# Performance work log

Measured on AMD Instinct MI355X. Metric: run time of the kernel, lower is better.

Reference implementation:

```python
import jax, jax.numpy as jnp
import numpy as np

B, L, D = 8192, 200, 64
NUM_ITEMS = 100000
HID = 64  # attention hidden_dim


def setup_inputs() -> dict:
    key = jax.random.key(0)
    ks = jax.random.split(key, 16)
    inp = {
        "item_sequence": jax.random.randint(ks[0], (B, L), 0, NUM_ITEMS),
        "click_sequence": jax.random.randint(ks[1], (B, L), 0, 2),
        "seq_length": jax.random.randint(ks[2], (B, 1), 1, L + 1),
        "target_item": jax.random.randint(ks[3], (B, 1), 0, NUM_ITEMS),
        "context_features": jax.random.normal(ks[4], (B, 9), dtype=jnp.float32),
        # embedding table (num_items+1, D)
        "emb_table": jax.random.normal(ks[5], (NUM_ITEMS + 1, D), dtype=jnp.float32) * 0.05,
        # attention MLP: Linear(2D->64), Linear(64->32), Linear(32->1)
        "aw1": jax.random.normal(ks[6], (2 * D, HID), dtype=jnp.float32) * 0.05,
        "ab1": jnp.zeros((HID,), jnp.float32),
        "aw2": jax.random.normal(ks[7], (HID, HID // 2), dtype=jnp.float32) * 0.05,
        "ab2": jnp.zeros((HID // 2,), jnp.float32),
        "aw3": jax.random.normal(ks[8], (HID // 2, 1), dtype=jnp.float32) * 0.05,
        "ab3": jnp.zeros((1,), jnp.float32),
        # context MLP: Linear(9->32)
        "cw": jax.random.normal(ks[9], (9, 32), dtype=jnp.float32) * 0.05,
        "cb": jnp.zeros((32,), jnp.float32),
        # head MLP: Linear(160->128), Linear(128->64), Linear(64->1)
        "mw1": jax.random.normal(ks[10], (2 * D + 32, 128), dtype=jnp.float32) * 0.05,
        "mb1": jnp.zeros((128,), jnp.float32),
        "mw2": jax.random.normal(ks[11], (128, 64), dtype=jnp.float32) * 0.05,
        "mb2": jnp.zeros((64,), jnp.float32),
        "mw3": jax.random.normal(ks[12], (64, 1), dtype=jnp.float32) * 0.05,
        "mb3": jnp.zeros((1,), jnp.float32),
    }
    return inp


def reference(item_sequence, click_sequence, seq_length, target_item, context_features,
              emb_table, aw1, ab1, aw2, ab2, aw3, ab3, cw, cb,
              mw1, mb1, mw2, mb2, mw3, mb3):
    seq_emb = emb_table[item_sequence]                 # [B, L, D]
    tgt_emb = emb_table[target_item[:, 0]]             # [B, D]
    seq_len = item_sequence.shape[1]
    mask = (jnp.arange(seq_len)[None, :] < seq_length).astype(seq_emb.dtype)  # [B, L]

    # DIN attention: concat(query, keys) -> 3-layer MLP -> masked softmax -> weighted sum
    q = jnp.broadcast_to(tgt_emb[:, None, :], seq_emb.shape)          # [B, L, D]
    att_in = jnp.concatenate([q, seq_emb], axis=-1)                   # [B, L, 2D]
    h = jax.nn.relu(att_in @ aw1 + ab1)
    h = jax.nn.relu(h @ aw2 + ab2)
    scores = (h @ aw3 + ab3)[..., 0]                                  # [B, L]
    scores = jnp.where(mask == 0, jnp.asarray(-1e9, scores.dtype), scores)
    w = jax.nn.softmax(scores, axis=1)                                # [B, L]
    attended = jnp.einsum('bl,bld->bd', w, seq_emb)                   # [B, D]

    ctx = jax.nn.relu(context_features @ cw + cb)                     # [B, 32]
    comb = jnp.concatenate([attended, tgt_emb, ctx], axis=1)          # [B, 2D+32]
    h = jax.nn.relu(comb @ mw1 + mb1)
    h = jax.nn.relu(h @ mw2 + mb2)
    out = jax.nn.sigmoid(h @ mw3 + mb3)[:, 0]                         # [B]
    return out
```

## Files before the change

kernel.cpp:

```cpp
#include <hip/hip_runtime.h>
#include <cmath>

typedef __attribute__((ext_vector_type(8))) short s16x8;
typedef __attribute__((ext_vector_type(4))) short s16x4;
typedef __attribute__((ext_vector_type(4))) float f32x4;

__device__ __forceinline__ short f2bf(float f) {
    union { float f; unsigned u; } v; v.f = f;
    unsigned r = v.u + 0x7FFFu + ((v.u >> 16) & 1u);
    return (short)(r >> 16);
}
__device__ __forceinline__ float bf2f(short s) {
    union { unsigned u; float f; } v; v.u = ((unsigned)(unsigned short)s) << 16;
    return v.f;
}
__device__ __forceinline__ s16x8 cvt8(float4 a, float4 b) {
    s16x8 r = { f2bf(a.x), f2bf(a.y), f2bf(a.z), f2bf(a.w),
                f2bf(b.x), f2bf(b.y), f2bf(b.z), f2bf(b.w) };
    return r;
}

#define W1SEQ_SH  0
#define W1TOP_SH  4096
#define W2_SH     8192
#define MW1T_SH   10240
#define MW2T_SH   30720
#define QC_F      19456
#define CB_SH     1087488

__global__ __launch_bounds__(256)
void din_wprep_kernel(const float* __restrict__ aw1,
                      const float* __restrict__ aw2,
                      const float* __restrict__ mw1,
                      const float* __restrict__ mw2,
                      short* __restrict__ ws)
{
    const int wb = blockIdx.x;
    const int t = threadIdx.x;
    if (wb == 0) {
        for (int idx = t; idx < 4096; idx += 256) {
            int j = idx & 7, lane = (idx >> 3) & 63, fr = idx >> 9;
            int n = (fr >> 1) * 16 + (lane & 15);
            int k = (fr & 1) * 32 + (lane >> 4) * 8 + j;
            ws[W1SEQ_SH + idx] = f2bf(aw1[(64 + k) * 64 + n]);
        }
    } else if (wb == 1) {
        for (int idx = t; idx < 4096; idx += 256) {
            int j = idx & 7, lane = (idx >> 3) & 63, fr = idx >> 9;
            int n = (fr >> 1) * 16 + (lane & 15);
            int k = (fr & 1) * 32 + (lane >> 4) * 8 + j;
            ws[W1TOP_SH + idx] = f2bf(aw1[k * 64 + n]);
        }
    } else if (wb == 2) {
        for (int idx = t; idx < 2048; idx += 256) {
            int j = idx & 7, lane = (idx >> 3) & 63, fr = idx >> 9;
            int n = (fr >> 1) * 16 + (lane & 15);
            int k = (fr & 1) * 32 + (lane >> 4) * 8 + j;
            ws[W2_SH + idx] = f2bf(aw2[k * 32 + n]);
        }
    } else if (wb == 3) {
        for (int idx = t; idx < 8192; idx += 256) {
            int j = idx & 7, lane = (idx >> 3) & 63, fr = idx >> 9;
            int n = (fr >> 2) * 16 + (lane & 15);
            int k = (fr & 3) * 32 + (lane >> 4) * 8 + j;
            ws[MW2T_SH + idx] = f2bf(mw2[k * 64 + n]);
        }
    } else {
        const int base = (wb - 4) * 5120;
        for (int ii = t; ii < 5120; ii += 256) {
            int idx = base + ii;
            int j = idx & 7, lane = (idx >> 3) & 63, fr = idx >> 9;
            int nt = fr / 5, ks = fr - nt * 5;
            int n = nt * 16 + (lane & 15);
            int k = ks * 32 + (lane >> 4) * 8 + j;
            ws[MW1T_SH + idx] = f2bf(mw1[k * 128 + n]);
        }
    }
}

__global__ __launch_bounds__(256)
void din_qc_kernel(const int* __restrict__ tgt_item,
                   const float* __restrict__ emb,
                   const float* __restrict__ ab1,
                   short* __restrict__ ws)
{
    const int t = threadIdx.x, lane = t & 63, wave = t >> 6;
    const int quad = lane >> 4, r16 = lane & 15;
    const short* w1t = ws + W1TOP_SH;
    float* qc = (float*)ws + QC_F;

    const int b0 = (blockIdx.x * 4 + wave) * 16;
    const int it = tgt_item[b0 + r16];
    const float* rp = emb + it * 64 + quad * 8;
    float4 v0 = *(const float4*)(rp),      v1 = *(const float4*)(rp + 4);
    float4 v2 = *(const float4*)(rp + 32), v3 = *(const float4*)(rp + 36);
    s16x8 a0 = cvt8(v0, v1);
    s16x8 a1 = cvt8(v2, v3);

    f32x4 acc[4] = {{0,0,0,0},{0,0,0,0},{0,0,0,0},{0,0,0,0}};
    #pragma unroll
    for (int nt = 0; nt < 4; ++nt) {
        s16x8 b_0 = *(const s16x8*)(w1t + ((nt * 2 + 0) * 64 + lane) * 8);
        s16x8 b_1 = *(const s16x8*)(w1t + ((nt * 2 + 1) * 64 + lane) * 8);
        acc[nt] = __builtin_amdgcn_mfma_f32_16x16x32_bf16(a0, b_0, acc[nt], 0, 0, 0);
        acc[nt] = __builtin_amdgcn_mfma_f32_16x16x32_bf16(a1, b_1, acc[nt], 0, 0, 0);
    }
    #pragma unroll
    for (int nt = 0; nt < 4; ++nt) {
        float bias = ab1[nt * 16 + r16];
        #pragma unroll
        for (int rr = 0; rr < 4; ++rr)
            qc[(b0 + quad * 4 + rr) * 64 + nt * 16 + r16] = acc[nt][rr] + bias;
    }
}

#define H1_PITCH 72
__global__ __launch_bounds__(256)
void din_att_v3(const int* __restrict__ item_seq,
                const int* __restrict__ seq_len_p,
                const int* __restrict__ tgt_item,
                const float* __restrict__ ctx_feat,
                const float* __restrict__ emb,
                const float* __restrict__ ab2,
                const float* __restrict__ aw3, const float* __restrict__ ab3,
                const float* __restrict__ cw,  const float* __restrict__ cb,
                short* __restrict__ ws)
{
    const int t = threadIdx.x, lane = t & 63, wave = t >> 6;
    const int quad = lane >> 4, r16 = lane & 15;
    __shared__ short s_w1[4096];
    __shared__ short s_h1[4][16 * H1_PITCH];
    __shared__ float s_sc[4][64];
    __shared__ float s_pool[4][64];
    __shared__ float s_m[4], s_e[4];

    const int b   = blockIdx.x;
    const int len = seq_len_p[b];
    const int tgt = tgt_item[b];

    {
        const s16x8* src = (const s16x8*)(ws + W1SEQ_SH);
        s16x8* dst = (s16x8*)s_w1;
        dst[t]       = src[t];
        dst[t + 256] = src[t + 256];
    }

    bool act[4];
    s16x8 af[4][2];
    #pragma unroll
    for (int ci = 0; ci < 4; ++ci) {
        const int c = wave + ci * 4;
        act[ci] = (c < 13) && (c * 16 < len);
        if (act[ci]) {
            int r = c * 16 + r16; if (r > 199) r = 199;
            const int it = item_seq[b * 200 + r];
            const float* rp = emb + it * 64 + quad * 8;
            float4 v0 = *(const float4*)(rp),      v1 = *(const float4*)(rp + 4);
            float4 v2 = *(const float4*)(rp + 32), v3 = *(const float4*)(rp + 36);
            af[ci][0] = cvt8(v0, v1);
            af[ci][1] = cvt8(v2, v3);
        }
    }
    s16x8 w2r[4];
    #pragma unroll
    for (int fr = 0; fr < 4; ++fr)
        w2r[fr] = *(const s16x8*)(ws + W2_SH + (fr * 64 + lane) * 8);
    const float* qcp = (const float*)ws + QC_F + b * 64;
    float qcv[4];
    #pragma unroll
    for (int nt = 0; nt < 4; ++nt) qcv[nt] = qcp[nt * 16 + r16];
    const float bias2_lo = ab2[r16], bias2_hi = ab2[16 + r16];
    const float w3_lo    = aw3[r16], w3_hi    = aw3[16 + r16];
    const float b3       = ab3[0];
    __syncthreads();

    short* h1w = s_h1[wave];

    #pragma unroll
    for (int ci = 0; ci < 4; ++ci) {
        if (!act[ci]) continue;
        f32x4 acc[4] = {{0,0,0,0},{0,0,0,0},{0,0,0,0},{0,0,0,0}};
        #pragma unroll
        for (int nt = 0; nt < 4; ++nt) {
            s16x8 b_0 = *(const s16x8*)&s_w1[((nt * 2 + 0) * 64 + lane) * 8];
            s16x8 b_1 = *(const s16x8*)&s_w1[((nt * 2 + 1) * 64 + lane) * 8];
            acc[nt] = __builtin_amdgcn_mfma_f32_16x16x32_bf16(af[ci][0], b_0, acc[nt], 0, 0, 0);
            acc[nt] = __builtin_amdgcn_mfma_f32_16x16x32_bf16(af[ci][1], b_1, acc[nt], 0, 0, 0);
        }
        #pragma unroll
        for (int nt = 0; nt < 4; ++nt)
            #pragma unroll
            for (int rr = 0; rr < 4; ++rr) {
                float v = fmaxf(acc[nt][rr] + qcv[nt], 0.f);
                h1w[(quad * 4 + rr) * H1_PITCH + nt * 16 + r16] = f2bf(v);
            }
        __builtin_amdgcn_wave_barrier();

        s16x8 h0  = *(const s16x8*)&h1w[r16 * H1_PITCH + quad * 8];
        s16x8 h1v = *(const s16x8*)&h1w[r16 * H1_PITCH + 32 + quad * 8];
        f32x4 c2[2] = {{0,0,0,0},{0,0,0,0}};
        #pragma unroll
        for (int nt = 0; nt < 2; ++nt) {
            c2[nt] = __builtin_amdgcn_mfma_f32_16x16x32_bf16(h0,  w2r[nt * 2],     c2[nt], 0, 0, 0);
            c2[nt] = __builtin_amdgcn_mfma_f32_16x16x32_bf16(h1v, w2r[nt * 2 + 1], c2[nt], 0, 0, 0);
        }
        #pragma unroll
        for (int rr = 0; rr < 4; ++rr) {
            float p = fmaxf(c2[0][rr] + bias2_lo, 0.f) * w3_lo
                    + fmaxf(c2[1][rr] + bias2_hi, 0.f) * w3_hi;
            p += __shfl_xor(p, 8);
            p += __shfl_xor(p, 4);
            p += __shfl_xor(p, 2);
            p += __shfl_xor(p, 1);
            if (r16 == 0) s_sc[wave][ci * 16 + quad * 4 + rr] = p + b3;
        }
        __builtin_amdgcn_wave_barrier();
    }

    const int ci_l = lane >> 4;
    const int c_l  = wave + ci_l * 4;
    const int grow = c_l * 16 + r16;
    const bool valid = (c_l < 13) && (grow < len);
    float sc = valid ? s_sc[wave][lane] : -1e30f;
    float m = sc;
    #pragma unroll
    for (int off = 32; off; off >>= 1) m = fmaxf(m, __shfl_xor(m, off));
    float e = valid ? __expf(sc - m) : 0.f;
    #pragma unroll
    for (int off = 32; off; off >>= 1) e += __shfl_xor(e, off);

    float p[16];
    #pragma unroll
    for (int i = 0; i < 16; ++i) p[i] = 0.f;
    #pragma unroll
    for (int ci = 0; ci < 4; ++ci) {
        if (!act[ci]) continue;
        const int row = (wave + ci * 4) * 16 + r16;
        const float w = (row < len) ? __expf(s_sc[wave][ci * 16 + r16] - m) : 0.f;
        #pragma unroll
        for (int j = 0; j < 8; ++j) {
            p[j]     += w * bf2f(af[ci][0][j]);
            p[8 + j] += w * bf2f(af[ci][1][j]);
        }
    }
    #pragma unroll
    for (int i = 0; i < 16; ++i) {
        p[i] += __shfl_xor(p[i], 1);
        p[i] += __shfl_xor(p[i], 2);
        p[i] += __shfl_xor(p[i], 4);
        p[i] += __shfl_xor(p[i], 8);
    }
    if (r16 == 0) {
        #pragma unroll
        for (int j = 0; j < 8; ++j) {
            s_pool[wave][quad * 8 + j]      = p[j];
            s_pool[wave][32 + quad * 8 + j] = p[8 + j];
        }
    }
    if (lane == 0) { s_m[wave] = m; s_e[wave] = e; }
    __syncthreads();

    short* comb = ws + CB_SH + b * 160;
    if (t < 64) {
        float gm = fmaxf(fmaxf(s_m[0], s_m[1]), fmaxf(s_m[2], s_m[3]));
        float s0 = __expf(s_m[0] - gm), s1 = __expf(s_m[1] - gm);
        float s2 = __expf(s_m[2] - gm), s3 = __expf(s_m[3] - gm);
        float denom = s0 * s_e[0] + s1 * s_e[1] + s2 * s_e[2] + s3 * s_e[3];
        float pooled = s0 * s_pool[0][t] + s1 * s_pool[1][t]
                     + s2 * s_pool[2][t] + s3 * s_pool[3][t];
        comb[t] = f2bf(pooled / denom);
    } else if (t < 96) {
        const int j = t - 64;
        float a = cb[j];
        #pragma unroll
        for (int k = 0; k < 9; ++k) a += ctx_feat[b * 9 + k] * cw[k * 32 + j];
        comb[128 + j] = f2bf(fmaxf(a, 0.f));
    } else if (t < 160) {
        comb[64 + (t - 96)] = f2bf(emb[tgt * 64 + (t - 96)]);
    }
}

__global__ __launch_bounds__(64)
void din_mlp_kernel(const float* __restrict__ mb1,
                    const float* __restrict__ mb2,
                    const float* __restrict__ mw3, const float* __restrict__ mb3,
                    const short* __restrict__ ws,
                    float* __restrict__ out)
{
    const int lane = threadIdx.x & 63;
    const int quad = lane >> 4, r16 = lane & 15;
    __shared__ short s_h1[16 * 136];
    __shared__ short s_h2[16 * 72];

    const int b0 = blockIdx.x * 16;
    const short* comb = ws + CB_SH;
    const short* w1   = ws + MW1T_SH;
    const short* w2   = ws + MW2T_SH;

    s16x8 a[5];
    #pragma unroll
    for (int ks = 0; ks < 5; ++ks)
        a[ks] = *(const s16x8*)(comb + (b0 + r16) * 160 + ks * 32 + quad * 8);
    f32x4 acc[8] = {{0,0,0,0},{0,0,0,0},{0,0,0,0},{0,0,0,0},{0,0,0,0},{0,0,0,0},{0,0,0,0},{0,0,0,0}};
    #pragma unroll
    for (int nt = 0; nt < 8; ++nt)
        #pragma unroll
        for (int ks = 0; ks < 5; ++ks) {
            s16x8 bf = *(const s16x8*)(w1 + ((nt * 5 + ks) * 64 + lane) * 8);
            acc[nt] = __builtin_amdgcn_mfma_f32_16x16x32_bf16(a[ks], bf, acc[nt], 0, 0, 0);
        }
    #pragma unroll
    for (int nt = 0; nt < 8; ++nt) {
        float bias = mb1[nt * 16 + r16];
        #pragma unroll
        for (int rr = 0; rr < 4; ++rr)
            s_h1[(quad * 4 + rr) * 136 + nt * 16 + r16] = f2bf(fmaxf(acc[nt][rr] + bias, 0.f));
    }
    __builtin_amdgcn_wave_barrier();

    s16x8 a2[4];
    #pragma unroll
    for (int ks = 0; ks < 4; ++ks)
        a2[ks] = *(const s16x8*)&s_h1[r16 * 136 + ks * 32 + quad * 8];
    f32x4 acc2[4] = {{0,0,0,0},{0,0,0,0},{0,0,0,0},{0,0,0,0}};
    #pragma unroll
    for (int nt = 0; nt < 4; ++nt)
        #pragma unroll
        for (int ks = 0; ks < 4; ++ks) {
            s16x8 bf = *(const s16x8*)(w2 + ((nt * 4 + ks) * 64 + lane) * 8);
            acc2[nt] = __builtin_amdgcn_mfma_f32_16x16x32_bf16(a2[ks], bf, acc2[nt], 0, 0, 0);
        }
    #pragma unroll
    for (int nt = 0; nt < 4; ++nt) {
        float bias = mb2[nt * 16 + r16];
        #pragma unroll
        for (int rr = 0; rr < 4; ++rr)
            s_h2[(quad * 4 + rr) * 72 + nt * 16 + r16] = f2bf(fmaxf(acc2[nt][rr] + bias, 0.f));
    }
    __builtin_amdgcn_wave_barrier();

    float p = 0.f;
    #pragma unroll
    for (int j = 0; j < 16; ++j)
        p += bf2f(s_h2[r16 * 72 + quad * 16 + j]) * mw3[quad * 16 + j];
    p += __shfl_xor(p, 16);
    p += __shfl_xor(p, 32);
    if (quad == 0) out[b0 + r16] = 1.f / (1.f + __expf(-(p + mb3[0])));
}

extern "C" void kernel_launch(void* const* d_in, const int* in_sizes, int n_in,
                              void* d_out, int out_size, void* d_ws, size_t ws_size,
                              hipStream_t stream)
{
    const int*   item_seq  = (const int*)  d_in[0];
    const int*   seq_len   = (const int*)  d_in[2];
    const int*   tgt_item  = (const int*)  d_in[3];
    const float* ctx_feat  = (const float*)d_in[4];
    const float* emb       = (const float*)d_in[5];
    const float* aw1 = (const float*)d_in[6];
    const float* ab1 = (const float*)d_in[7];
    const float* aw2 = (const float*)d_in[8];
    const float* ab2 = (const float*)d_in[9];
    const float* aw3 = (const float*)d_in[10];
    const float* ab3 = (const float*)d_in[11];
    const float* cw  = (const float*)d_in[12];
    const float* cb  = (const float*)d_in[13];
    const float* mw1 = (const float*)d_in[14];
    const float* mb1 = (const float*)d_in[15];
    const float* mw2 = (const float*)d_in[16];
    const float* mb2 = (const float*)d_in[17];
    const float* mw3 = (const float*)d_in[18];
    const float* mb3 = (const float*)d_in[19];
    float* out = (float*)d_out;
    short* ws  = (short*)d_ws;

    hipLaunchKernelGGL(din_wprep_kernel, dim3(8), dim3(256), 0, stream,
                       aw1, aw2, mw1, mw2, ws);
    hipLaunchKernelGGL(din_qc_kernel, dim3(128), dim3(256), 0, stream,
                       tgt_item, emb, ab1, ws);
    hipLaunchKernelGGL(din_att_v3, dim3(8192), dim3(256), 0, stream,
                       item_seq, seq_len, tgt_item, ctx_feat, emb,
                       ab2, aw3, ab3, cw, cb, ws);
    hipLaunchKernelGGL(din_mlp_kernel, dim3(512), dim3(64), 0, stream,
                       mb1, mb2, mw3, mb3, ws, out);
}
```

Before: 193.2 us.

## Use packed bf16 conversion, spread weight prep and head MLP across more waves

```diff
diff --git a/kernel.cpp b/kernel.cpp
--- a/kernel.cpp
+++ b/kernel.cpp
@@ -14,10 +14,18 @@
     union { unsigned u; float f; } v; v.u = ((unsigned)(unsigned short)s) << 16;
     return v.f;
 }
+__device__ __forceinline__ unsigned cvtpk2(float lo, float hi) {
+    unsigned r;
+    asm("v_cvt_pk_bf16_f32 %0, %1, %2" : "=v"(r) : "v"(lo), "v"(hi));
+    return r;
+}
 __device__ __forceinline__ s16x8 cvt8(float4 a, float4 b) {
-    s16x8 r = { f2bf(a.x), f2bf(a.y), f2bf(a.z), f2bf(a.w),
-                f2bf(b.x), f2bf(b.y), f2bf(b.z), f2bf(b.w) };
-    return r;
+    union { s16x8 v; unsigned u[4]; } r;
+    r.u[0] = cvtpk2(a.x, a.y);
+    r.u[1] = cvtpk2(a.z, a.w);
+    r.u[2] = cvtpk2(b.x, b.y);
+    r.u[3] = cvtpk2(b.z, b.w);
+    return r.v;
 }
 
 #define W1SEQ_SH  0
@@ -35,39 +43,39 @@
                       const float* __restrict__ mw2,
                       short* __restrict__ ws)
 {
-    const int wb = blockIdx.x;
-    const int t = threadIdx.x;
-    if (wb == 0) {
-        for (int idx = t; idx < 4096; idx += 256) {
+    const int g  = blockIdx.x >> 3;
+    const int sb = blockIdx.x & 7;
+    const int t  = threadIdx.x;
+    if (g == 0) {
+        for (int idx = sb * 512 + t; idx < sb * 512 + 512; idx += 256) {
             int j = idx & 7, lane = (idx >> 3) & 63, fr = idx >> 9;
             int n = (fr >> 1) * 16 + (lane & 15);
             int k = (fr & 1) * 32 + (lane >> 4) * 8 + j;
             ws[W1SEQ_SH + idx] = f2bf(aw1[(64 + k) * 64 + n]);
         }
-    } else if (wb == 1) {
-        for (int idx = t; idx < 4096; idx += 256) {
+    } else if (g == 1) {
+        for (int idx = sb * 512 + t; idx < sb * 512 + 512; idx += 256) {
             int j = idx & 7, lane = (idx >> 3) & 63, fr = idx >> 9;
             int n = (fr >> 1) * 16 + (lane & 15);
             int k = (fr & 1) * 32 + (lane >> 4) * 8 + j;
             ws[W1TOP_SH + idx] = f2bf(aw1[k * 64 + n]);
         }
-    } else if (wb == 2) {
-        for (int idx = t; idx < 2048; idx += 256) {
-            int j = idx & 7, lane = (idx >> 3) & 63, fr = idx >> 9;
-            int n = (fr >> 1) * 16 + (lane & 15);
-            int k = (fr & 1) * 32 + (lane >> 4) * 8 + j;
-            ws[W2_SH + idx] = f2bf(aw2[k * 32 + n]);
-        }
-    } else if (wb == 3) {
-        for (int idx = t; idx < 8192; idx += 256) {
+    } else if (g == 2) {
+        int idx = sb * 256 + t;
+        int j = idx & 7, lane = (idx >> 3) & 63, fr = idx >> 9;
+        int n = (fr >> 1) * 16 + (lane & 15);
+        int k = (fr & 1) * 32 + (lane >> 4) * 8 + j;
+        ws[W2_SH + idx] = f2bf(aw2[k * 32 + n]);
+    } else if (g == 3) {
+        for (int idx = sb * 1024 + t; idx < sb * 1024 + 1024; idx += 256) {
             int j = idx & 7, lane = (idx >> 3) & 63, fr = idx >> 9;
             int n = (fr >> 2) * 16 + (lane & 15);
             int k = (fr & 3) * 32 + (lane >> 4) * 8 + j;
             ws[MW2T_SH + idx] = f2bf(mw2[k * 64 + n]);
         }
     } else {
-        const int base = (wb - 4) * 5120;
-        for (int ii = t; ii < 5120; ii += 256) {
+        const int base = ((g - 4) * 8 + sb) * 640;
+        for (int ii = t; ii < 640; ii += 256) {
             int idx = base + ii;
             int j = idx & 7, lane = (idx >> 3) & 63, fr = idx >> 9;
             int nt = fr / 5, ks = fr - nt * 5;
@@ -188,12 +196,18 @@
             acc[nt] = __builtin_amdgcn_mfma_f32_16x16x32_bf16(af[ci][1], b_1, acc[nt], 0, 0, 0);
         }
         #pragma unroll
-        for (int nt = 0; nt < 4; ++nt)
-            #pragma unroll
-            for (int rr = 0; rr < 4; ++rr) {
-                float v = fmaxf(acc[nt][rr] + qcv[nt], 0.f);
-                h1w[(quad * 4 + rr) * H1_PITCH + nt * 16 + r16] = f2bf(v);
-            }
+        for (int nt = 0; nt < 4; ++nt) {
+            float v0 = fmaxf(acc[nt][0] + qcv[nt], 0.f);
+            float v1 = fmaxf(acc[nt][1] + qcv[nt], 0.f);
+            float v2 = fmaxf(acc[nt][2] + qcv[nt], 0.f);
+            float v3 = fmaxf(acc[nt][3] + qcv[nt], 0.f);
+            unsigned p01 = cvtpk2(v0, v1), p23 = cvtpk2(v2, v3);
+            const int col = nt * 16 + r16;
+            h1w[(quad * 4 + 0) * H1_PITCH + col] = (short)p01;
+            h1w[(quad * 4 + 1) * H1_PITCH + col] = (short)(p01 >> 16);
+            h1w[(quad * 4 + 2) * H1_PITCH + col] = (short)p23;
+            h1w[(quad * 4 + 3) * H1_PITCH + col] = (short)(p23 >> 16);
+        }
         __builtin_amdgcn_wave_barrier();
 
         s16x8 h0  = *(const s16x8*)&h1w[r16 * H1_PITCH + quad * 8];
@@ -280,14 +294,14 @@
     }
 }
 
-__global__ __launch_bounds__(64)
+__global__ __launch_bounds__(256)
 void din_mlp_kernel(const float* __restrict__ mb1,
                     const float* __restrict__ mb2,
                     const float* __restrict__ mw3, const float* __restrict__ mb3,
                     const short* __restrict__ ws,
                     float* __restrict__ out)
 {
-    const int lane = threadIdx.x & 63;
+    const int t = threadIdx.x, lane = t & 63, wave = t >> 6;
     const int quad = lane >> 4, r16 = lane & 15;
     __shared__ short s_h1[16 * 136];
     __shared__ short s_h2[16 * 72];
@@ -301,51 +315,68 @@
     #pragma unroll
     for (int ks = 0; ks < 5; ++ks)
         a[ks] = *(const s16x8*)(comb + (b0 + r16) * 160 + ks * 32 + quad * 8);
-    f32x4 acc[8] = {{0,0,0,0},{0,0,0,0},{0,0,0,0},{0,0,0,0},{0,0,0,0},{0,0,0,0},{0,0,0,0},{0,0,0,0}};
-    #pragma unroll
-    for (int nt = 0; nt < 8; ++nt)
+    f32x4 acc[2] = {{0,0,0,0},{0,0,0,0}};
+    #pragma unroll
+    for (int ntl = 0; ntl < 2; ++ntl) {
+        const int nt = wave * 2 + ntl;
         #pragma unroll
         for (int ks = 0; ks < 5; ++ks) {
             s16x8 bf = *(const s16x8*)(w1 + ((nt * 5 + ks) * 64 + lane) * 8);
-            acc[nt] = __builtin_amdgcn_mfma_f32_16x16x32_bf16(a[ks], bf, acc[nt], 0, 0, 0);
-        }
-    #pragma unroll
-    for (int nt = 0; nt < 8; ++nt) {
+            acc[ntl] = __builtin_amdgcn_mfma_f32_16x16x32_bf16(a[ks], bf, acc[ntl], 0, 0, 0);
+        }
+    }
+    #pragma unroll
+    for (int ntl = 0; ntl < 2; ++ntl) {
+        const int nt = wave * 2 + ntl;
         float bias = mb1[nt * 16 + r16];
-        #pragma unroll
-        for (int rr = 0; rr < 4; ++rr)
-            s_h1[(quad * 4 + rr) * 136 + nt * 16 + r16] = f2bf(fmaxf(acc[nt][rr] + bias, 0.f));
-    }
-    __builtin_amdgcn_wave_barrier();
+        float v0 = fmaxf(acc[ntl][0] + bias, 0.f);
+        float v1 = fmaxf(acc[ntl][1] + bias, 0.f);
+        float v2 = fmaxf(acc[ntl][2] + bias, 0.f);
+        float v3 = fmaxf(acc[ntl][3] + bias, 0.f);
+        unsigned p01 = cvtpk2(v0, v1), p23 = cvtpk2(v2, v3);
+        const int col = nt * 16 + r16;
+        s_h1[(quad * 4 + 0) * 136 + col] = (short)p01;
+        s_h1[(quad * 4 + 1) * 136 + col] = (short)(p01 >> 16);
+        s_h1[(quad * 4 + 2) * 136 + col] = (short)p23;
+        s_h1[(quad * 4 + 3) * 136 + col] = (short)(p23 >> 16);
+    }
+    __syncthreads();
 
     s16x8 a2[4];
     #pragma unroll
     for (int ks = 0; ks < 4; ++ks)
         a2[ks] = *(const s16x8*)&s_h1[r16 * 136 + ks * 32 + quad * 8];
-    f32x4 acc2[4] = {{0,0,0,0},{0,0,0,0},{0,0,0,0},{0,0,0,0}};
-    #pragma unroll
-    for (int nt = 0; nt < 4; ++nt)
+    f32x4 acc2 = {0,0,0,0};
+    {
+        const int nt = wave;
         #pragma unroll
         for (int ks = 0; ks < 4; ++ks) {
             s16x8 bf = *(const s16x8*)(w2 + ((nt * 4 + ks) * 64 + lane) * 8);
-            acc2[nt] = __builtin_amdgcn_mfma_f32_16x16x32_bf16(a2[ks], bf, acc2[nt], 0, 0, 0);
-        }
-    #pragma unroll
-    for (int nt = 0; nt < 4; ++nt) {
+            acc2 = __builtin_amdgcn_mfma_f32_16x16x32_bf16(a2[ks], bf, acc2, 0, 0, 0);
+        }
         float bias = mb2[nt * 16 + r16];
-        #pragma unroll
-        for (int rr = 0; rr < 4; ++rr)
-            s_h2[(quad * 4 + rr) * 72 + nt * 16 + r16] = f2bf(fmaxf(acc2[nt][rr] + bias, 0.f));
-    }
-    __builtin_amdgcn_wave_barrier();
-
-    float p = 0.f;
-    #pragma unroll
-    for (int j = 0; j < 16; ++j)
-        p += bf2f(s_h2[r16 * 72 + quad * 16 + j]) * mw3[quad * 16 + j];
-    p += __shfl_xor(p, 16);
-    p += __shfl_xor(p, 32);
-    if (quad == 0) out[b0 + r16] = 1.f / (1.f + __expf(-(p + mb3[0])));
+        float v0 = fmaxf(acc2[0] + bias, 0.f);
+        float v1 = fmaxf(acc2[1] + bias, 0.f);
+        float v2 = fmaxf(acc2[2] + bias, 0.f);
+        float v3 = fmaxf(acc2[3] + bias, 0.f);
+        unsigned p01 = cvtpk2(v0, v1), p23 = cvtpk2(v2, v3);
+        const int col = nt * 16 + r16;
+        s_h2[(quad * 4 + 0) * 72 + col] = (short)p01;
+        s_h2[(quad * 4 + 1) * 72 + col] = (short)(p01 >> 16);
+        s_h2[(quad * 4 + 2) * 72 + col] = (short)p23;
+        s_h2[(quad * 4 + 3) * 72 + col] = (short)(p23 >> 16);
+    }
+    __syncthreads();
+
+    if (wave == 0) {
+        float p = 0.f;
+        #pragma unroll
+        for (int j = 0; j < 16; ++j)
+            p += bf2f(s_h2[r16 * 72 + quad * 16 + j]) * mw3[quad * 16 + j];
+        p += __shfl_xor(p, 16);
+        p += __shfl_xor(p, 32);
+        if (quad == 0) out[b0 + r16] = 1.f / (1.f + __expf(-(p + mb3[0])));
+    }
 }
 
 extern "C" void kernel_launch(void* const* d_in, const int* in_sizes, int n_in,
@@ -374,13 +405,13 @@
     float* out = (float*)d_out;
     short* ws  = (short*)d_ws;
 
-    hipLaunchKernelGGL(din_wprep_kernel, dim3(8), dim3(256), 0, stream,
+    hipLaunchKernelGGL(din_wprep_kernel, dim3(64), dim3(256), 0, stream,
                        aw1, aw2, mw1, mw2, ws);
     hipLaunchKernelGGL(din_qc_kernel, dim3(128), dim3(256), 0, stream,
                        tgt_item, emb, ab1, ws);
     hipLaunchKernelGGL(din_att_v3, dim3(8192), dim3(256), 0, stream,
                        item_seq, seq_len, tgt_item, ctx_feat, emb,
                        ab2, aw3, ab3, cw, cb, ws);
-    hipLaunchKernelGGL(din_mlp_kernel, dim3(512), dim3(64), 0, stream,
+    hipLaunchKernelGGL(din_mlp_kernel, dim3(512), dim3(256), 0, stream,
                        mb1, mb2, mw3, mb3, ws, out);
 }
```

Result: faster. 188.8 us (-2.3%).
